# Kernel tuning notes

Hardware: AMD Instinct MI355X
Metric: run time of the kernel (lower is better)

The kernel has to match this reference:

```python
import jax, jax.numpy as jnp
import numpy as np

B, T, D, M = 16, 4096, 256, 1024


def setup_inputs() -> dict:
    key = jax.random.key(0)
    kx, ke = jax.random.split(key)
    x = jax.random.normal(kx, (B, T, D), dtype=jnp.float32)
    init_bound = 1.0 / M
    embedding = jax.random.uniform(ke, (M, D), dtype=jnp.float32,
                                   minval=-init_bound, maxval=init_bound)
    return {"x": x, "embedding": embedding}


def reference(x, embedding):
    bsz, tsz, d = x.shape
    m = embedding.shape[0]
    x_flat = jax.lax.stop_gradient(x).reshape(-1, d)  # [N, D]

    distances = (jnp.sum(embedding ** 2, axis=1)[None, :]
                 + jnp.sum(x_flat ** 2, axis=1, keepdims=True)
                 - 2.0 * (x_flat @ embedding.T))  # [N, M]
    indices = jnp.argmin(distances.astype(jnp.float32), axis=-1)  # [N]

    quantized = embedding[indices].reshape(bsz, tsz, d)

    # usage stats via scatter-add (avoids materializing NxM one-hot)
    n = indices.shape[0]
    counts = jnp.zeros((m,), dtype=jnp.float32).at[indices].add(1.0)
    used_curr = jnp.sum((counts >= 1.0).astype(jnp.float32))
    avg_probs = counts / n
    perplexity = jnp.exp(-jnp.sum(avg_probs * jnp.log(avg_probs + 1e-10)))

    commitment_loss = jnp.mean((x - jax.lax.stop_gradient(quantized)) ** 2)

    # straight-through estimator
    quantized_st = x + jax.lax.stop_gradient(quantized - x)

    quantization_inds = indices.reshape(bsz, tsz, 1)
    return (quantized_st, quantization_inds, used_curr, perplexity, commitment_loss)
```

## Files before the change

### kernel.cpp

```cpp
#include <hip/hip_runtime.h>
#include <float.h>
#include <stdint.h>

#define N_TOK   65536
#define DIM     256
#define M_CODES 1024
#define CHUNK_CODES 32
#define N_CHUNKS (M_CODES / CHUNK_CODES)
#define CHUNK_BYTES 16384
#define BT      128
#define THR     2e-3f

typedef __attribute__((ext_vector_type(8))) short bf16x8;
typedef __attribute__((ext_vector_type(4))) float f32x4;

__device__ __forceinline__ unsigned short f2bf(float f) {
    unsigned u = __builtin_bit_cast(unsigned, f);
    unsigned r = (u + 0x7fffu + ((u >> 16) & 1u)) >> 16;
    return (unsigned short)r;
}

__device__ __forceinline__ void gload_lds16(const void* g, void* l) {
    __builtin_amdgcn_global_load_lds(
        (const __attribute__((address_space(1))) unsigned int*)g,
        (__attribute__((address_space(3))) unsigned int*)l, 16, 0, 0);
}

__global__ void prep_emb_kernel(const float* __restrict__ emb,
                                unsigned short* __restrict__ eb,
                                float* __restrict__ e2) {
    const int gid  = blockIdx.x * blockDim.x + threadIdx.x;
    const int code = gid >> 6;
    const int lane = gid & 63;
    if (code >= M_CODES) return;
    const float4 v = *reinterpret_cast<const float4*>(emb + (size_t)code * DIM + lane * 4);
    float s = __fmul_rn(v.x, v.x);
    s = __fadd_rn(s, __fmul_rn(v.y, v.y));
    s = __fadd_rn(s, __fmul_rn(v.z, v.z));
    s = __fadd_rn(s, __fmul_rn(v.w, v.w));
    #pragma unroll
    for (int off = 32; off; off >>= 1) s = __fadd_rn(s, __shfl_xor(s, off));

    const int d0 = lane * 4;
    const int chunk = code >> 5, ct = (code >> 4) & 1, cl = code & 15;
    const int kk = d0 >> 5, g = (d0 >> 3) & 3, j = d0 & 7;
    ushort4 b4;
    b4.x = f2bf(v.x); b4.y = f2bf(v.y); b4.z = f2bf(v.z); b4.w = f2bf(v.w);
    const size_t dst = (size_t)chunk * CHUNK_BYTES + (size_t)(kk * 2 + ct) * 1024
                     + (size_t)(g * 16 + cl) * 16 + (size_t)j * 2;
    *reinterpret_cast<ushort4*>(reinterpret_cast<char*>(eb) + dst) = b4;
    if (lane == 0) e2[code] = s;
}

__global__ __launch_bounds__(256, 2) void prefilter_kernel(
    const float* __restrict__ x, const unsigned short* __restrict__ eb,
    const float* __restrict__ e2, unsigned int* __restrict__ cand)
{
    __shared__ char smem[2 * CHUNK_BYTES + 4096];
    float* e2s = reinterpret_cast<float*>(smem + 2 * CHUNK_BYTES);

    const int tid  = threadIdx.x;
    const int w    = tid >> 6, lane = tid & 63;
    const int cl   = lane & 15, g = lane >> 4;
    const int t0   = blockIdx.x * BT;

    e2s[tid]       = e2[tid];
    e2s[tid + 256] = e2[tid + 256];
    e2s[tid + 512] = e2[tid + 512];
    e2s[tid + 768] = e2[tid + 768];

    {
        const char* src = reinterpret_cast<const char*>(eb) + (size_t)tid * 16;
        #pragma unroll
        for (int p = 0; p < 4; ++p)
            gload_lds16(src + p * 4096, smem + p * 4096 + tid * 16);
    }

    bf16x8 afr[2][8];
    #pragma unroll
    for (int rt = 0; rt < 2; ++rt) {
        const float* xrow = x + (size_t)(t0 + w * 32 + rt * 16 + cl) * DIM + g * 8;
        #pragma unroll
        for (int kk = 0; kk < 8; ++kk) {
            const float4 lo = *reinterpret_cast<const float4*>(xrow + kk * 32);
            const float4 hi = *reinterpret_cast<const float4*>(xrow + kk * 32 + 4);
            bf16x8 a;
            a[0] = (short)f2bf(lo.x); a[1] = (short)f2bf(lo.y);
            a[2] = (short)f2bf(lo.z); a[3] = (short)f2bf(lo.w);
            a[4] = (short)f2bf(hi.x); a[5] = (short)f2bf(hi.y);
            a[6] = (short)f2bf(hi.z); a[7] = (short)f2bf(hi.w);
            afr[rt][kk] = a;
        }
    }

    float    tv0[8], tv1[8];
    unsigned ti0[8], ti1[8];
    #pragma unroll
    for (int r = 0; r < 8; ++r) { tv0[r] = FLT_MAX; tv1[r] = FLT_MAX; ti0[r] = 0; ti1[r] = 0; }

    asm volatile("s_waitcnt vmcnt(0)");
    __syncthreads();

    for (int chunk = 0; chunk < N_CHUNKS; ++chunk) {
        char* cb_ = smem + ((chunk & 1) ? CHUNK_BYTES : 0);
        char* nb_ = smem + ((chunk & 1) ? 0 : CHUNK_BYTES);
        if (chunk + 1 < N_CHUNKS) {
            const char* src = reinterpret_cast<const char*>(eb)
                            + (size_t)(chunk + 1) * CHUNK_BYTES + (size_t)tid * 16;
            #pragma unroll
            for (int p = 0; p < 4; ++p)
                gload_lds16(src + p * 4096, nb_ + p * 4096 + tid * 16);
        }

        const f32x4 z = {0.0f, 0.0f, 0.0f, 0.0f};
        f32x4 acc[2][2];
        acc[0][0] = z; acc[0][1] = z; acc[1][0] = z; acc[1][1] = z;

        #pragma unroll
        for (int kk = 0; kk < 8; ++kk) {
            #pragma unroll
            for (int ct = 0; ct < 2; ++ct) {
                const bf16x8 b = *reinterpret_cast<const bf16x8*>(
                    cb_ + ((kk * 2 + ct) << 10) + lane * 16);
                acc[0][ct] = __builtin_amdgcn_mfma_f32_16x16x32_bf16(afr[0][kk], b, acc[0][ct], 0, 0, 0);
                acc[1][ct] = __builtin_amdgcn_mfma_f32_16x16x32_bf16(afr[1][kk], b, acc[1][ct], 0, 0, 0);
            }
        }

        const int cbase = chunk * CHUNK_CODES;
        #pragma unroll
        for (int ct = 0; ct < 2; ++ct) {
            const unsigned code = (unsigned)(cbase + ct * 16 + cl);
            const float e2v = e2s[code];
            #pragma unroll
            for (int rt = 0; rt < 2; ++rt)
                #pragma unroll
                for (int q = 0; q < 4; ++q) {
                    const float c = e2v - 2.0f * acc[rt][ct][q];
                    const int r = rt * 4 + q;
                    if (c < tv1[r]) {
                        if (c < tv0[r]) { tv1[r] = tv0[r]; ti1[r] = ti0[r]; tv0[r] = c; ti0[r] = code; }
                        else            { tv1[r] = c; ti1[r] = code; }
                    }
                }
        }
        __syncthreads();
    }

    float*    mv = reinterpret_cast<float*>(smem);
    unsigned* mi = reinterpret_cast<unsigned*>(smem + 16896);
    #pragma unroll
    for (int r = 0; r < 8; ++r) {
        const int rt = r >> 2, q = r & 3;
        const int row = w * 32 + rt * 16 + g * 4 + q;
        mv[row * 33 + cl * 2 + 0] = tv0[r];  mi[row * 33 + cl * 2 + 0] = ti0[r];
        mv[row * 33 + cl * 2 + 1] = tv1[r];  mi[row * 33 + cl * 2 + 1] = ti1[r];
    }
    __syncthreads();
    if (tid < BT) {
        const float*    v  = mv + tid * 33;
        const unsigned* ii = mi + tid * 33;
        float vmin = v[0]; unsigned imin = ii[0];
        for (int j2 = 1; j2 < 32; ++j2) {
            const float vv = v[j2]; const unsigned ij = ii[j2];
            if (vv < vmin || (vv == vmin && ij < imin)) { vmin = vv; imin = ij; }
        }
        unsigned lst[7]; lst[0] = imin; int cnt = 1;
        const float lim = vmin + THR;
        for (int j2 = 0; j2 < 32; ++j2) {
            const unsigned ij = ii[j2];
            if (v[j2] <= lim && ij != imin && cnt < 7) lst[cnt++] = ij;
        }
        unsigned* cp = cand + (size_t)(t0 + tid) * 8;
        cp[0] = (unsigned)cnt;
        #pragma unroll
        for (int j2 = 0; j2 < 7; ++j2) cp[1 + j2] = (j2 < cnt) ? lst[j2] : imin;
    }
}

__global__ __launch_bounds__(256) void rescue_kernel(
    const float* __restrict__ x, const float* __restrict__ emb,
    const float* __restrict__ e2, const unsigned* __restrict__ cand,
    float* __restrict__ out_q, float* __restrict__ out_inds,
    unsigned* __restrict__ counts, float* __restrict__ cparts)
{
    const int tid = threadIdx.x, w = tid >> 6, lane = tid & 63;
    const int t = blockIdx.x * 4 + w;

    const float4 xv = *reinterpret_cast<const float4*>(x + (size_t)t * DIM + lane * 4);
    float s = __fmul_rn(xv.x, xv.x);
    s = __fadd_rn(s, __fmul_rn(xv.y, xv.y));
    s = __fadd_rn(s, __fmul_rn(xv.z, xv.z));
    s = __fadd_rn(s, __fmul_rn(xv.w, xv.w));
    #pragma unroll
    for (int off = 32; off; off >>= 1) s = __fadd_rn(s, __shfl_xor(s, off));
    const float x2t = s;

    const unsigned* cp = cand + (size_t)t * 8;
    const int cnt = min((int)cp[0], 7);
    float bd = FLT_MAX; unsigned bi = 0xFFFFFFFFu;
    for (int cix = 0; cix < cnt; ++cix) {
        const unsigned ci = cp[1 + cix];
        const float4 ev = *reinterpret_cast<const float4*>(emb + (size_t)ci * DIM + lane * 4);
        float p = __fmul_rn(xv.x, ev.x);
        p = fmaf(xv.y, ev.y, p);
        p = fmaf(xv.z, ev.z, p);
        p = fmaf(xv.w, ev.w, p);
        #pragma unroll
        for (int off = 32; off; off >>= 1) p = __fadd_rn(p, __shfl_xor(p, off));
        const float d = __fsub_rn(__fadd_rn(e2[ci], x2t), __fmul_rn(2.0f, p));
        if (d < bd || (d == bd && ci < bi)) { bd = d; bi = ci; }
    }

    const float4 qv = *reinterpret_cast<const float4*>(emb + (size_t)bi * DIM + lane * 4);
    float4 o;
    o.x = __fadd_rn(xv.x, __fsub_rn(qv.x, xv.x));
    o.y = __fadd_rn(xv.y, __fsub_rn(qv.y, xv.y));
    o.z = __fadd_rn(xv.z, __fsub_rn(qv.z, xv.z));
    o.w = __fadd_rn(xv.w, __fsub_rn(qv.w, xv.w));
    *reinterpret_cast<float4*>(out_q + (size_t)t * DIM + lane * 4) = o;

    float cl2 = 0.0f, dx;
    dx = __fsub_rn(xv.x, qv.x); cl2 = fmaf(dx, dx, cl2);
    dx = __fsub_rn(xv.y, qv.y); cl2 = fmaf(dx, dx, cl2);
    dx = __fsub_rn(xv.z, qv.z); cl2 = fmaf(dx, dx, cl2);
    dx = __fsub_rn(xv.w, qv.w); cl2 = fmaf(dx, dx, cl2);
    #pragma unroll
    for (int off = 32; off; off >>= 1) cl2 += __shfl_xor(cl2, off);

    __shared__ float wp[4];
    if (lane == 0) {
        out_inds[t] = (float)bi;
        atomicAdd(&counts[bi], 1u);
        wp[w] = cl2;
    }
    __syncthreads();
    if (tid == 0) cparts[blockIdx.x] = (wp[0] + wp[1]) + (wp[2] + wp[3]);
}

__global__ void stats_kernel(const unsigned* __restrict__ counts,
                             const float* __restrict__ cparts,
                             float* __restrict__ out)
{
    const int tid = threadIdx.x, lane = tid & 63, wv = tid >> 6;
    const float c = (float)counts[tid];
    float u = (c >= 1.0f) ? 1.0f : 0.0f;
    const float p = c / 65536.0f;
    float e = p * logf(p + 1e-10f);
    double cs = 0.0;
    #pragma unroll
    for (int j = 0; j < 16; ++j) cs += (double)cparts[tid * 16 + j];
    #pragma unroll
    for (int off = 32; off; off >>= 1) {
        u  += __shfl_xor(u, off);
        e  += __shfl_xor(e, off);
        cs += __shfl_xor(cs, off);
    }
    __shared__ float  su[16], se[16];
    __shared__ double sc[16];
    if (lane == 0) { su[wv] = u; se[wv] = e; sc[wv] = cs; }
    __syncthreads();
    if (tid == 0) {
        float U = 0.0f, E = 0.0f; double C = 0.0;
        for (int wj = 0; wj < 16; ++wj) { U += su[wj]; E += se[wj]; C += sc[wj]; }
        out[16842752] = U;
        out[16842753] = expf(-E);
        out[16842754] = (float)(C / 16777216.0);
    }
}

extern "C" void kernel_launch(void* const* d_in, const int* in_sizes, int n_in,
                              void* d_out, int out_size, void* d_ws, size_t ws_size,
                              hipStream_t stream) {
    const float* x   = (const float*)d_in[0];
    const float* emb = (const float*)d_in[1];
    float* out = (float*)d_out;

    char* ws = (char*)d_ws;
    float*          e2     = (float*)ws;
    unsigned short* eb     = (unsigned short*)(ws + 4096);
    unsigned*       cand   = (unsigned*)(ws + 528384);
    unsigned*       counts = (unsigned*)(ws + 2625536);
    float*          cparts = (float*)(ws + 2629632);

    float* out_q    = out;
    float* out_inds = out + 16777216;

    hipMemsetAsync(counts, 0, 4096, stream);

    prep_emb_kernel<<<256, 256, 0, stream>>>(emb, eb, e2);
    prefilter_kernel<<<N_TOK / BT, 256, 0, stream>>>(x, eb, e2, cand);
    rescue_kernel<<<N_TOK / 4, 256, 0, stream>>>(x, emb, e2, cand, out_q, out_inds, counts, cparts);
    stats_kernel<<<1, 1024, 0, stream>>>(counts, cparts, out);
}
```

Measured before the change: 228.7 us.

## Triple-buffer codebook chunks, skip rescue for single candidates, fold memset into prep

The prefilter kernel moves from double to triple buffering of codebook chunks in LDS. Each iteration waits on a partial vmcnt with a single barrier, so loads run two chunks ahead and the trailing per-chunk syncthreads goes away. The rescue kernel skips the exact fp32 distance recomputation when the prefilter found only one candidate, and the memset of counts is folded into prep_emb_kernel to drop one launch. The LDS use grows by one chunk per block, which may affect occupancy at two blocks per CU.

```diff
diff --git a/kernel.cpp b/kernel.cpp
--- a/kernel.cpp
+++ b/kernel.cpp
@@ -28,8 +28,10 @@
 
 __global__ void prep_emb_kernel(const float* __restrict__ emb,
                                 unsigned short* __restrict__ eb,
-                                float* __restrict__ e2) {
+                                float* __restrict__ e2,
+                                unsigned* __restrict__ counts) {
     const int gid  = blockIdx.x * blockDim.x + threadIdx.x;
+    if (gid < M_CODES) counts[gid] = 0u;
     const int code = gid >> 6;
     const int lane = gid & 63;
     if (code >= M_CODES) return;
@@ -56,24 +58,23 @@
     const float* __restrict__ x, const unsigned short* __restrict__ eb,
     const float* __restrict__ e2, unsigned int* __restrict__ cand)
 {
-    __shared__ char smem[2 * CHUNK_BYTES + 4096];
-    float* e2s = reinterpret_cast<float*>(smem + 2 * CHUNK_BYTES);
+    __shared__ char smem[3 * CHUNK_BYTES + 4096];
+    float* e2s = reinterpret_cast<float*>(smem + 3 * CHUNK_BYTES);
 
     const int tid  = threadIdx.x;
     const int w    = tid >> 6, lane = tid & 63;
     const int cl   = lane & 15, g = lane >> 4;
     const int t0   = blockIdx.x * BT;
 
-    e2s[tid]       = e2[tid];
-    e2s[tid + 256] = e2[tid + 256];
-    e2s[tid + 512] = e2[tid + 512];
-    e2s[tid + 768] = e2[tid + 768];
-
     {
-        const char* src = reinterpret_cast<const char*>(eb) + (size_t)tid * 16;
+        const char* s0 = reinterpret_cast<const char*>(eb) + (size_t)tid * 16;
         #pragma unroll
         for (int p = 0; p < 4; ++p)
-            gload_lds16(src + p * 4096, smem + p * 4096 + tid * 16);
+            gload_lds16(s0 + p * 4096, smem + p * 4096 + tid * 16);
+        const char* s1 = s0 + CHUNK_BYTES;
+        #pragma unroll
+        for (int p = 0; p < 4; ++p)
+            gload_lds16(s1 + p * 4096, smem + CHUNK_BYTES + p * 4096 + tid * 16);
     }
 
     bf16x8 afr[2][8];
@@ -93,29 +94,25 @@
         }
     }
 
+    e2s[tid]       = e2[tid];
+    e2s[tid + 256] = e2[tid + 256];
+    e2s[tid + 512] = e2[tid + 512];
+    e2s[tid + 768] = e2[tid + 768];
+    asm volatile("s_waitcnt lgkmcnt(0)" ::: "memory");
+
     float    tv0[8], tv1[8];
     unsigned ti0[8], ti1[8];
     #pragma unroll
     for (int r = 0; r < 8; ++r) { tv0[r] = FLT_MAX; tv1[r] = FLT_MAX; ti0[r] = 0; ti1[r] = 0; }
 
-    asm volatile("s_waitcnt vmcnt(0)");
-    __syncthreads();
-
-    for (int chunk = 0; chunk < N_CHUNKS; ++chunk) {
-        char* cb_ = smem + ((chunk & 1) ? CHUNK_BYTES : 0);
-        char* nb_ = smem + ((chunk & 1) ? 0 : CHUNK_BYTES);
-        if (chunk + 1 < N_CHUNKS) {
-            const char* src = reinterpret_cast<const char*>(eb)
-                            + (size_t)(chunk + 1) * CHUNK_BYTES + (size_t)tid * 16;
-            #pragma unroll
-            for (int p = 0; p < 4; ++p)
-                gload_lds16(src + p * 4096, nb_ + p * 4096 + tid * 16);
-        }
-
+    char* bA = smem;
+    char* bB = smem + CHUNK_BYTES;
+    char* bC = smem + 2 * CHUNK_BYTES;
+
+    auto compute = [&](int chunk, const char* cb_) {
         const f32x4 z = {0.0f, 0.0f, 0.0f, 0.0f};
         f32x4 acc[2][2];
         acc[0][0] = z; acc[0][1] = z; acc[1][0] = z; acc[1][1] = z;
-
         #pragma unroll
         for (int kk = 0; kk < 8; ++kk) {
             #pragma unroll
@@ -126,7 +123,6 @@
                 acc[1][ct] = __builtin_amdgcn_mfma_f32_16x16x32_bf16(afr[1][kk], b, acc[1][ct], 0, 0, 0);
             }
         }
-
         const int cbase = chunk * CHUNK_CODES;
         #pragma unroll
         for (int ct = 0; ct < 2; ++ct) {
@@ -144,8 +140,29 @@
                     }
                 }
         }
-        __syncthreads();
-    }
+    };
+
+    for (int chunk = 0; chunk < N_CHUNKS - 1; ++chunk) {
+        asm volatile("s_waitcnt vmcnt(4)" ::: "memory");
+        __builtin_amdgcn_s_barrier();
+        __builtin_amdgcn_sched_barrier(0);
+        if (chunk + 2 < N_CHUNKS) {
+            const char* src = reinterpret_cast<const char*>(eb)
+                            + (size_t)(chunk + 2) * CHUNK_BYTES + (size_t)tid * 16;
+            #pragma unroll
+            for (int p = 0; p < 4; ++p)
+                gload_lds16(src + p * 4096, bC + p * 4096 + tid * 16);
+        }
+        __builtin_amdgcn_sched_barrier(0);
+        compute(chunk, bA);
+        char* t_ = bA; bA = bB; bB = bC; bC = t_;
+    }
+    asm volatile("s_waitcnt vmcnt(0)" ::: "memory");
+    __builtin_amdgcn_s_barrier();
+    __builtin_amdgcn_sched_barrier(0);
+    compute(N_CHUNKS - 1, bA);
+
+    __syncthreads();
 
     float*    mv = reinterpret_cast<float*>(smem);
     unsigned* mi = reinterpret_cast<unsigned*>(smem + 16896);
@@ -188,28 +205,35 @@
     const int t = blockIdx.x * 4 + w;
 
     const float4 xv = *reinterpret_cast<const float4*>(x + (size_t)t * DIM + lane * 4);
-    float s = __fmul_rn(xv.x, xv.x);
-    s = __fadd_rn(s, __fmul_rn(xv.y, xv.y));
-    s = __fadd_rn(s, __fmul_rn(xv.z, xv.z));
-    s = __fadd_rn(s, __fmul_rn(xv.w, xv.w));
-    #pragma unroll
-    for (int off = 32; off; off >>= 1) s = __fadd_rn(s, __shfl_xor(s, off));
-    const float x2t = s;
 
     const unsigned* cp = cand + (size_t)t * 8;
-    const int cnt = min((int)cp[0], 7);
-    float bd = FLT_MAX; unsigned bi = 0xFFFFFFFFu;
-    for (int cix = 0; cix < cnt; ++cix) {
-        const unsigned ci = cp[1 + cix];
-        const float4 ev = *reinterpret_cast<const float4*>(emb + (size_t)ci * DIM + lane * 4);
-        float p = __fmul_rn(xv.x, ev.x);
-        p = fmaf(xv.y, ev.y, p);
-        p = fmaf(xv.z, ev.z, p);
-        p = fmaf(xv.w, ev.w, p);
-        #pragma unroll
-        for (int off = 32; off; off >>= 1) p = __fadd_rn(p, __shfl_xor(p, off));
-        const float d = __fsub_rn(__fadd_rn(e2[ci], x2t), __fmul_rn(2.0f, p));
-        if (d < bd || (d == bd && ci < bi)) { bd = d; bi = ci; }
+    const int cnt = (int)cp[0];
+    unsigned bi;
+    if (cnt == 1) {
+        bi = cp[1];
+    } else {
+        float s = __fmul_rn(xv.x, xv.x);
+        s = __fadd_rn(s, __fmul_rn(xv.y, xv.y));
+        s = __fadd_rn(s, __fmul_rn(xv.z, xv.z));
+        s = __fadd_rn(s, __fmul_rn(xv.w, xv.w));
+        #pragma unroll
+        for (int off = 32; off; off >>= 1) s = __fadd_rn(s, __shfl_xor(s, off));
+        const float x2t = s;
+
+        const int cn = min(cnt, 7);
+        float bd = FLT_MAX; bi = 0xFFFFFFFFu;
+        for (int cix = 0; cix < cn; ++cix) {
+            const unsigned ci = cp[1 + cix];
+            const float4 ev = *reinterpret_cast<const float4*>(emb + (size_t)ci * DIM + lane * 4);
+            float p = __fmul_rn(xv.x, ev.x);
+            p = fmaf(xv.y, ev.y, p);
+            p = fmaf(xv.z, ev.z, p);
+            p = fmaf(xv.w, ev.w, p);
+            #pragma unroll
+            for (int off = 32; off; off >>= 1) p = __fadd_rn(p, __shfl_xor(p, off));
+            const float d = __fsub_rn(__fadd_rn(e2[ci], x2t), __fmul_rn(2.0f, p));
+            if (d < bd || (d == bd && ci < bi)) { bd = d; bi = ci; }
+        }
     }
 
     const float4 qv = *reinterpret_cast<const float4*>(emb + (size_t)bi * DIM + lane * 4);
@@ -286,9 +310,7 @@
     float* out_q    = out;
     float* out_inds = out + 16777216;
 
-    hipMemsetAsync(counts, 0, 4096, stream);
-
-    prep_emb_kernel<<<256, 256, 0, stream>>>(emb, eb, e2);
+    prep_emb_kernel<<<256, 256, 0, stream>>>(emb, eb, e2, counts);
     prefilter_kernel<<<N_TOK / BT, 256, 0, stream>>>(x, eb, e2, cand);
     rescue_kernel<<<N_TOK / 4, 256, 0, stream>>>(x, emb, e2, cand, out_q, out_inds, counts, cparts);
     stats_kernel<<<1, 1024, 0, stream>>>(counts, cparts, out);
```

New measurement: 213.6 us. 6.6% less time.
